# Kernel tuning notes

Hardware: AMD Instinct MI355X
Metric: run time of the kernel (lower is better)

The kernel has to match this reference:

```python
import jax, jax.numpy as jnp
import numpy as np

VOCAB, EMB, HID, LAT = 32000, 512, 1024, 512
B, T = 32, 128


def setup_inputs() -> dict:
    key = jax.random.key(0)
    ks = jax.random.split(key, 10)
    s = 0.02
    return {
        "latent_vector": jax.random.normal(ks[0], (B, LAT), jnp.float32),
        "target_tokens": jax.random.randint(ks[1], (B, T), 0, VOCAB),
        "emb": jax.random.normal(ks[2], (VOCAB, EMB), jnp.float32) * s,
        "W_lh": jax.random.normal(ks[3], (HID, LAT), jnp.float32) * s,
        "b_lh": jnp.zeros((HID,), jnp.float32),
        "W_ih": jax.random.normal(ks[4], (4 * HID, EMB), jnp.float32) * s,
        "b_ih": jnp.zeros((4 * HID,), jnp.float32),
        "W_hh": jax.random.normal(ks[5], (4 * HID, HID), jnp.float32) * s,
        "b_hh": jnp.zeros((4 * HID,), jnp.float32),
        "W_out": jax.random.normal(ks[6], (VOCAB, HID), jnp.float32) * s,
        "b_out": jnp.zeros((VOCAB,), jnp.float32),
    }


def reference(latent_vector, target_tokens, emb, W_lh, b_lh, W_ih, b_ih, W_hh, b_hh, W_out, b_out):
    # teacher_forcing_ratio = 1.0 (deterministic): input at step t is target_tokens[:, t-1]
    h = latent_vector @ W_lh.T + b_lh            # [B, HID]
    c = jnp.zeros_like(h)
    xs = emb[target_tokens[:, :-1]]              # [B, T-1, EMB]
    xs = jnp.swapaxes(xs, 0, 1)                  # [T-1, B, EMB]

    def step(carry, x):
        h, c = carry
        gates = x @ W_ih.T + b_ih + h @ W_hh.T + b_hh   # [B, 4*HID]
        i, f, g, o = jnp.split(gates, 4, axis=-1)       # PyTorch LSTM gate order
        c = jax.nn.sigmoid(f) * c + jax.nn.sigmoid(i) * jnp.tanh(g)
        h = jax.nn.sigmoid(o) * jnp.tanh(c)
        logits = h @ W_out.T + b_out                    # [B, VOCAB]
        return (h, c), logits

    _, logits = jax.lax.scan(step, (h, c), xs)          # [T-1, B, VOCAB]
    return jnp.swapaxes(logits, 0, 1)                   # [B, T-1, VOCAB]
```

## Files before the change

kernel.cpp:

```cpp
#include <hip/hip_runtime.h>
#include <cstdint>

typedef __bf16 bf16x8 __attribute__((ext_vector_type(8)));
typedef __bf16 bf16x4 __attribute__((ext_vector_type(4)));
typedef float  f32x4  __attribute__((ext_vector_type(4)));

#define VOCAB 32000
#define EMB   512
#define HID   1024
#define LAT   512
#define BATCH 32
#define TSTEP 127
#define MROWS 4064
#define MPAD  4096
#define G4    4096
#define NBLK2 64
#define NTM   32
#define NTN   250
#define FSTRIDE 64

__device__ __forceinline__ float sigf(float x){ return 1.0f / (1.0f + __expf(-x)); }
__device__ __forceinline__ float tanhfast(float x){
    float ax = fabsf(x);
    float e  = __expf(-2.0f * ax);
    float t  = (1.0f - e) / (1.0f + e);
    return copysignf(t, x);
}

__device__ __forceinline__ void gll16(void* lds, const void* gsrc){
    __builtin_amdgcn_global_load_lds(
        (const __attribute__((address_space(1))) unsigned int*)gsrc,
        (__attribute__((address_space(3))) unsigned int*)lds,
        16, 0, 0);
}

__global__ __launch_bounds__(256) void init_kernel(
    const float* __restrict__ latent,
    const float* __restrict__ Wlh,
    const float* __restrict__ blh,
    __bf16* __restrict__ h0,
    __bf16* __restrict__ Hall,
    unsigned* __restrict__ flags,
    const float* __restrict__ Whh,
    __bf16* __restrict__ Whhb)
{
    if (blockIdx.x >= 128){
        const int n4 = G4 * HID / 4;
        for (int i = (blockIdx.x - 128) * 256 + threadIdx.x; i < n4; i += 64 * 256){
            float4 v = ((const float4*)Whh)[i];
            bf16x4 o = { (__bf16)v.x, (__bf16)v.y, (__bf16)v.z, (__bf16)v.w };
            ((bf16x4*)Whhb)[i] = o;
        }
        return;
    }
    if (blockIdx.x == 0 && threadIdx.x < 128)
        flags[threadIdx.x * FSTRIDE] = 0u;

    int id = blockIdx.x * 256 + threadIdx.x;
    int b = id >> 10, j = id & 1023;
    float s = blh[j];
    const float4* lr = (const float4*)(latent + (size_t)b * LAT);
    const float4* wr = (const float4*)(Wlh + (size_t)j * LAT);
    for (int k = 0; k < LAT / 4; ++k){
        float4 a = lr[k], w = wr[k];
        s += a.x * w.x + a.y * w.y + a.z * w.z + a.w * w.w;
    }
    h0[id] = (__bf16)s;
    Hall[(size_t)MROWS * HID + id] = (__bf16)0.0f;
}

__global__ __launch_bounds__(256) void gemm_xg(
    const float* __restrict__ emb,
    const float* __restrict__ Wih,
    const int*   __restrict__ tok,
    float*       __restrict__ xg,
    const float* __restrict__ bih,
    const float* __restrict__ bhh)
{
    __shared__ __bf16 As[2][128 * 32];
    __shared__ __bf16 Bs[2][128 * 32];

    const int tid  = threadIdx.x;
    const int wid  = tid >> 6, lane = tid & 63;
    const int tile_n = blockIdx.x, tile_m = blockIdx.y;
    const int wr = wid >> 1, wc = wid & 1;

    f32x4 acc[4][4] = {};

    auto stage = [&](int kt, int buf){
        #pragma unroll
        for (int j = 0; j < 2; ++j){
            const int slot = tid + j * 256;
            const int row  = slot >> 2;
            const int kb   = kt * 32 + (slot & 3) * 8;
            {
                const int brow = tile_n * 128 + row;
                const float4* p = (const float4*)(Wih + (size_t)brow * EMB + kb);
                float4 u = p[0], v = p[1];
                bf16x8 w = { (__bf16)u.x, (__bf16)u.y, (__bf16)u.z, (__bf16)u.w,
                             (__bf16)v.x, (__bf16)v.y, (__bf16)v.z, (__bf16)v.w };
                *(bf16x8*)&Bs[buf][row * 32 + (slot & 3) * 8] = w;
            }
            {
                int r = tile_m * 128 + row;
                int rc = (r < MROWS) ? r : (MROWS - 1);
                int token = tok[(rc & 31) * 128 + (rc >> 5)];
                const float4* p = (const float4*)(emb + (size_t)token * EMB + kb);
                float4 u = p[0], v = p[1];
                bf16x8 w = { (__bf16)u.x, (__bf16)u.y, (__bf16)u.z, (__bf16)u.w,
                             (__bf16)v.x, (__bf16)v.y, (__bf16)v.z, (__bf16)v.w };
                *(bf16x8*)&As[buf][row * 32 + (slot & 3) * 8] = w;
            }
        }
    };

    const int KT = EMB / 32;
    stage(0, 0);
    for (int kt = 0; kt < KT; ++kt){
        const int buf = kt & 1;
        __syncthreads();
        if (kt + 1 < KT) stage(kt + 1, buf ^ 1);
        const __bf16* Abuf = As[buf];
        const __bf16* Bbuf = Bs[buf];
        const int ar = lane & 15, ko = (lane >> 4) * 8;
        bf16x8 av[4], bv[4];
        #pragma unroll
        for (int m = 0; m < 4; ++m)
            av[m] = *(const bf16x8*)&Abuf[(wr * 64 + m * 16 + ar) * 32 + ko];
        #pragma unroll
        for (int n = 0; n < 4; ++n)
            bv[n] = *(const bf16x8*)&Bbuf[(wc * 64 + n * 16 + ar) * 32 + ko];
        #pragma unroll
        for (int m = 0; m < 4; ++m)
            #pragma unroll
            for (int n = 0; n < 4; ++n)
                acc[m][n] = __builtin_amdgcn_mfma_f32_16x16x32_bf16(av[m], bv[n], acc[m][n], 0, 0, 0);
    }

    const int r0 = tile_m * 128 + wr * 64 + ((lane >> 4) << 2);
    const int c0 = tile_n * 128 + wc * 64 + (lane & 15);
    #pragma unroll
    for (int m = 0; m < 4; ++m){
        #pragma unroll
        for (int n = 0; n < 4; ++n){
            const int col = c0 + n * 16;
            float badd = bih[col] + bhh[col];
            #pragma unroll
            for (int q = 0; q < 4; ++q){
                int row = r0 + m * 16 + q;
                xg[(size_t)row * G4 + col] = acc[m][n][q] + badd;
            }
        }
    }
}

template<int BF16B>
__global__ __launch_bounds__(256) void gemm_logits(
    const __bf16* __restrict__ A,
    const float*  __restrict__ Bf,
    const __bf16* __restrict__ Bb,
    float*        __restrict__ C,
    const float*  __restrict__ bias)
{
    __shared__ __bf16 As[2][128 * 32];
    __shared__ __bf16 Bs[2][128 * 32];

    const int tid  = threadIdx.x;
    const int wid  = tid >> 6, lane = tid & 63;
    const int bid = blockIdx.x;
    const int s   = (bid & 7) * (NTM * NTN / 8) + (bid >> 3);
    const int g   = s / (8 * NTN), rem = s % (8 * NTN);
    const int tile_m = g * 8 + (rem & 7);
    const int tile_n = rem >> 3;
    const int wr = wid >> 1, wc = wid & 1;

    f32x4 acc[4][4] = {};

    auto stage = [&](int kt, int buf){
        const int kb = kt * 32 + (lane & 3) * 8;
        #pragma unroll
        for (int c2 = 0; c2 < 2; ++c2){
            int rA = tile_m * 128 + c2 * 64 + wid * 16 + (lane >> 2);
            gll16(&As[buf][c2 * 2048 + wid * 512], A + (size_t)rA * HID + kb);
            if constexpr (BF16B){
                int rB = tile_n * 128 + c2 * 64 + wid * 16 + (lane >> 2);
                gll16(&Bs[buf][c2 * 2048 + wid * 512], Bb + (size_t)rB * HID + kb);
            }
        }
        if constexpr (!BF16B){
            #pragma unroll
            for (int j = 0; j < 2; ++j){
                const int slot = tid + j * 256;
                const int row  = slot >> 2;
                const int kb2  = kt * 32 + (slot & 3) * 8;
                const int brow = tile_n * 128 + row;
                const float4* p = (const float4*)(Bf + (size_t)brow * HID + kb2);
                float4 u = p[0], v = p[1];
                bf16x8 w = { (__bf16)u.x, (__bf16)u.y, (__bf16)u.z, (__bf16)u.w,
                             (__bf16)v.x, (__bf16)v.y, (__bf16)v.z, (__bf16)v.w };
                *(bf16x8*)&Bs[buf][row * 32 + (slot & 3) * 8] = w;
            }
        }
    };

    const int KT = HID / 32;
    stage(0, 0);
    for (int kt = 0; kt < KT; ++kt){
        const int buf = kt & 1;
        __syncthreads();
        if (kt + 1 < KT) stage(kt + 1, buf ^ 1);
        const __bf16* Abuf = As[buf];
        const __bf16* Bbuf = Bs[buf];
        const int ar = lane & 15, ko = (lane >> 4) * 8;
        bf16x8 av[4], bv[4];
        #pragma unroll
        for (int m = 0; m < 4; ++m)
            av[m] = *(const bf16x8*)&Abuf[(wr * 64 + m * 16 + ar) * 32 + ko];
        #pragma unroll
        for (int n = 0; n < 4; ++n)
            bv[n] = *(const bf16x8*)&Bbuf[(wc * 64 + n * 16 + ar) * 32 + ko];
        #pragma unroll
        for (int m = 0; m < 4; ++m)
            #pragma unroll
            for (int n = 0; n < 4; ++n)
                acc[m][n] = __builtin_amdgcn_mfma_f32_16x16x32_bf16(
                    bv[n], av[m], acc[m][n], 0, 0, 0);
    }

    const int r0 = tile_m * 128 + wr * 64 + (lane & 15);
    const int c0 = tile_n * 128 + wc * 64 + ((lane >> 4) << 2);
    #pragma unroll
    for (int m = 0; m < 4; ++m){
        const int row = r0 + m * 16;
        if (row < MROWS){
            const int t = row >> 5, b = row & 31;
            float* crow = &C[((size_t)b * TSTEP + t) * VOCAB];
            #pragma unroll
            for (int n = 0; n < 4; ++n){
                const int col = c0 + n * 16;
                const f32x4 bd = *(const f32x4*)&bias[col];
                f32x4 v = acc[m][n] + bd;
                __builtin_nontemporal_store(v, (f32x4*)&crow[col]);
            }
        }
    }
}

__global__ __launch_bounds__(512) void lstm_coop(
    const float*  __restrict__ xg,
    __bf16*       __restrict__ Hall,
    __bf16*       __restrict__ hbuf,
    const __bf16* __restrict__ Whhb,
    unsigned*     __restrict__ flags,
    const float*  __restrict__ Woutf,
    __bf16*       __restrict__ Woutb)
{
    if (blockIdx.x >= NBLK2){
        if (Woutb){
            const int n4 = VOCAB * HID / 4;
            for (int i = (blockIdx.x - NBLK2) * 512 + threadIdx.x; i < n4; i += 192 * 512){
                float4 v = ((const float4*)Woutf)[i];
                bf16x4 o = { (__bf16)v.x, (__bf16)v.y, (__bf16)v.z, (__bf16)v.w };
                ((bf16x4*)Woutb)[i] = o;
            }
        }
        return;
    }

    __shared__ float lds_g[8 * 8 * 4 * 64];
    const int tid = threadIdx.x, wid = tid >> 6, lane = tid & 63;
    const int jb = blockIdx.x * 16;

    bf16x8 bfrag[4][4];
    {
        const int un = lane & 15, ko = (lane >> 4) * 8;
        #pragma unroll
        for (int cf = 0; cf < 4; ++cf){
            const __bf16* base =
                Whhb + ((size_t)cf * HID + jb + un) * HID + wid * 128 + ko;
            #pragma unroll
            for (int ks = 0; ks < 4; ++ks)
                bfrag[cf][ks] = *(const bf16x8*)(base + ks * 32);
        }
    }

    const int b2 = tid >> 3, up0 = (tid & 7) * 2;
    const int mt2 = b2 >> 4, r2 = b2 & 15, reg2 = r2 & 3, lb2 = (r2 >> 2) << 4;
    float cst[2] = {0.0f, 0.0f};

    const float* xq = xg + (size_t)b2 * G4 + jb + up0;
    float2 xv[4];
    if (tid < 256){
        #pragma unroll
        for (int g = 0; g < 4; ++g) xv[g] = *(const float2*)(xq + g * HID);
    }

    const size_t e0 = (size_t)(lane & 15) * HID + wid * 128 + (lane >> 4) * 8;
    const int pflag = (wid * 8 + (lane & 7)) * FSTRIDE;

    for (int t = 0; t < TSTEP; ++t){
        if (t > 0){
            const unsigned tgt = (unsigned)t;
            for (;;){
                unsigned f = __hip_atomic_load(&flags[pflag],
                                __ATOMIC_RELAXED, __HIP_MEMORY_SCOPE_AGENT);
                if (f >= tgt) break;
                __builtin_amdgcn_s_sleep(1);
            }
        }

        const unsigned long long* hq =
            (const unsigned long long*)(hbuf + (size_t)(t & 1) * (BATCH * HID));
        union { unsigned long long q[2]; bf16x8 v; } xa[8];
        #pragma unroll
        for (int ks = 0; ks < 4; ++ks){
            size_t q0 = (e0 + (size_t)ks * 32) >> 2;
            size_t q1 = q0 + ((size_t)16 * HID >> 2);
            xa[ks].q[0]     = __hip_atomic_load(hq + q0,     __ATOMIC_RELAXED, __HIP_MEMORY_SCOPE_AGENT);
            xa[ks].q[1]     = __hip_atomic_load(hq + q0 + 1, __ATOMIC_RELAXED, __HIP_MEMORY_SCOPE_AGENT);
            xa[4 + ks].q[0] = __hip_atomic_load(hq + q1,     __ATOMIC_RELAXED, __HIP_MEMORY_SCOPE_AGENT);
            xa[4 + ks].q[1] = __hip_atomic_load(hq + q1 + 1, __ATOMIC_RELAXED, __HIP_MEMORY_SCOPE_AGENT);
        }
        f32x4 a[2][4] = {};
        #pragma unroll
        for (int ks = 0; ks < 4; ++ks){
            #pragma unroll
            for (int cf = 0; cf < 4; ++cf){
                a[0][cf] = __builtin_amdgcn_mfma_f32_16x16x32_bf16(xa[ks].v,     bfrag[cf][ks], a[0][cf], 0, 0, 0);
                a[1][cf] = __builtin_amdgcn_mfma_f32_16x16x32_bf16(xa[4 + ks].v, bfrag[cf][ks], a[1][cf], 0, 0, 0);
            }
        }
        #pragma unroll
        for (int bh = 0; bh < 2; ++bh)
            #pragma unroll
            for (int cf = 0; cf < 4; ++cf)
                #pragma unroll
                for (int q = 0; q < 4; ++q)
                    lds_g[((((bh * 4 + cf) * 8 + wid) * 4) + q) * 64 + lane] = a[bh][cf][q];
        __syncthreads();

        unsigned pku = 0;
        if (tid < 256){
            const float* xn = xq + (size_t)(t + 1) * (BATCH * G4);
            float2 xnew[4];
            #pragma unroll
            for (int g = 0; g < 4; ++g) xnew[g] = *(const float2*)(xn + g * HID);

            float h2[2];
            #pragma unroll
            for (int du = 0; du < 2; ++du){
                int u2 = up0 + du;
                float gate[4];
                #pragma unroll
                for (int ty = 0; ty < 4; ++ty){
                    int li = lb2 | u2;
                    float s = 0.0f;
                    #pragma unroll
                    for (int w = 0; w < 8; ++w)
                        s += lds_g[((((mt2 * 4 + ty) * 8 + w) * 4) + reg2) * 64 + li];
                    gate[ty] = s;
                }
                float gi = gate[0] + ((du == 0) ? xv[0].x : xv[0].y);
                float gf = gate[1] + ((du == 0) ? xv[1].x : xv[1].y);
                float gc = gate[2] + ((du == 0) ? xv[2].x : xv[2].y);
                float go = gate[3] + ((du == 0) ? xv[3].x : xv[3].y);
                float c = sigf(gf) * cst[du] + sigf(gi) * tanhfast(gc);
                cst[du] = c;
                h2[du] = sigf(go) * tanhfast(c);
            }
            #pragma unroll
            for (int g = 0; g < 4; ++g) xv[g] = xnew[g];

            union { __bf16 h[2]; unsigned u; } pk;
            pk.h[0] = (__bf16)h2[0]; pk.h[1] = (__bf16)h2[1];
            pku = pk.u;
            unsigned* hw = (unsigned*)(hbuf + (size_t)((t + 1) & 1) * (BATCH * HID)
                                       + (size_t)b2 * HID + jb + up0);
            __hip_atomic_store(hw, pku, __ATOMIC_RELAXED, __HIP_MEMORY_SCOPE_AGENT);
        }

        if (t + 1 == TSTEP){
            if (tid < 256)
                *(unsigned*)(Hall + ((size_t)t * BATCH + b2) * HID + jb + up0) = pku;
            break;
        }

        __syncthreads();
        if (tid == 0)
            __hip_atomic_store(&flags[blockIdx.x * FSTRIDE], (unsigned)(t + 1),
                               __ATOMIC_RELAXED, __HIP_MEMORY_SCOPE_AGENT);
        if (tid < 256)
            *(unsigned*)(Hall + ((size_t)t * BATCH + b2) * HID + jb + up0) = pku;
    }
}

extern "C" void kernel_launch(void* const* d_in, const int* in_sizes, int n_in,
                              void* d_out, int out_size, void* d_ws, size_t ws_size,
                              hipStream_t stream)
{
    const float* latent = (const float*)d_in[0];
    const int*   tokens = (const int*)d_in[1];
    const float* emb    = (const float*)d_in[2];
    const float* Wlh    = (const float*)d_in[3];
    const float* blh    = (const float*)d_in[4];
    const float* Wih    = (const float*)d_in[5];
    const float* bih    = (const float*)d_in[6];
    const float* Whh    = (const float*)d_in[7];
    const float* bhh    = (const float*)d_in[8];
    const float* Wout   = (const float*)d_in[9];
    const float* bout   = (const float*)d_in[10];
    float* out = (float*)d_out;

    const size_t xg_b   = (size_t)MPAD * G4 * 4;
    const size_t hall_b = (size_t)MPAD * HID * 2;
    const size_t whh_b  = (size_t)G4 * HID * 2;
    const size_t wout_b = (size_t)VOCAB * HID * 2;
    const size_t hb_b   = (size_t)2 * BATCH * HID * 2;
    const size_t cnt_b  = (size_t)128 * FSTRIDE * 4;

    char* p = (char*)d_ws;
    const bool wsA = ws_size >= xg_b + hall_b + whh_b + wout_b + hb_b + cnt_b;
    const bool wsB = ws_size >= hall_b + whh_b + wout_b + hb_b + cnt_b;

    float* xg;
    if (wsA){ xg = (float*)p; p += xg_b; }
    else    { xg = (float*)d_out; }
    __bf16* Hall = (__bf16*)p; p += hall_b;
    __bf16* Whhb = (__bf16*)p; p += whh_b;
    __bf16* Woutb = nullptr;
    if (wsA || wsB){ Woutb = (__bf16*)p; p += wout_b; }
    __bf16* hbuf = (__bf16*)p; p += hb_b;
    unsigned* flags = (unsigned*)p; p += cnt_b;

    init_kernel<<<dim3(192), dim3(256), 0, stream>>>(
        latent, Wlh, blh, hbuf, Hall, flags, Whh, Whhb);

    gemm_xg<<<dim3(G4 / 128, MPAD / 128), dim3(256), 0, stream>>>(
        emb, Wih, tokens, xg, bih, bhh);

    {
        const float*  xgc   = xg;
        __bf16*       hallp = Hall;
        __bf16*       hbp   = hbuf;
        const __bf16* whhp  = Whhb;
        unsigned*     flagp = flags;
        const float*  wof   = Wout;
        __bf16*       wob   = Woutb;
        void* args[] = { (void*)&xgc, (void*)&hallp, (void*)&hbp, (void*)&whhp,
                         (void*)&flagp, (void*)&wof, (void*)&wob };
        (void)hipLaunchCooperativeKernel((void*)lstm_coop, dim3(256), dim3(512),
                                         args, 0, stream);
    }

    if (Woutb)
        gemm_logits<1><<<dim3(NTM * NTN), dim3(256), 0, stream>>>(
            Hall, (const float*)nullptr, Woutb, out, bout);
    else
        gemm_logits<0><<<dim3(NTM * NTN), dim3(256), 0, stream>>>(
            Hall, Wout, (const __bf16*)nullptr, out, bout);
}
```

Before: 1.187 ms.

## Replace per-block step flags with tagged hidden-state words for LSTM sync

Result: slower. 1.774 ms (+49.5%).

```diff
diff --git a/kernel.cpp b/kernel.cpp
--- a/kernel.cpp
+++ b/kernel.cpp
@@ -17,7 +17,7 @@
 #define NBLK2 64
 #define NTM   32
 #define NTN   250
-#define FSTRIDE 64
+#define HWORDS 16384
 
 __device__ __forceinline__ float sigf(float x){ return 1.0f / (1.0f + __expf(-x)); }
 __device__ __forceinline__ float tanhfast(float x){
@@ -33,14 +33,14 @@
         (__attribute__((address_space(3))) unsigned int*)lds,
         16, 0, 0);
 }
+__device__ __forceinline__ void bar(){ asm volatile("s_barrier" ::: "memory"); }
 
 __global__ __launch_bounds__(256) void init_kernel(
     const float* __restrict__ latent,
     const float* __restrict__ Wlh,
     const float* __restrict__ blh,
-    __bf16* __restrict__ h0,
+    unsigned long long* __restrict__ hbt,
     __bf16* __restrict__ Hall,
-    unsigned* __restrict__ flags,
     const float* __restrict__ Whh,
     __bf16* __restrict__ Whhb)
 {
@@ -53,8 +53,6 @@
         }
         return;
     }
-    if (blockIdx.x == 0 && threadIdx.x < 128)
-        flags[threadIdx.x * FSTRIDE] = 0u;
 
     int id = blockIdx.x * 256 + threadIdx.x;
     int b = id >> 10, j = id & 1023;
@@ -65,7 +63,14 @@
         float4 a = lr[k], w = wr[k];
         s += a.x * w.x + a.y * w.y + a.z * w.z + a.w * w.w;
     }
-    h0[id] = (__bf16)s;
+    float s_hi = __shfl_down(s, 1);
+    if ((j & 1) == 0){
+        union { __bf16 h[2]; unsigned u; } pk;
+        pk.h[0] = (__bf16)s; pk.h[1] = (__bf16)s_hi;
+        hbt[(size_t)b * 512 + (j >> 1)] = (unsigned long long)pk.u;
+    }
+    if (id < HWORDS)
+        hbt[HWORDS + id] = 0xFFFFFFFF00000000ULL;
     Hall[(size_t)MROWS * HID + id] = (__bf16)0.0f;
 }
 
@@ -247,13 +252,12 @@
 }
 
 __global__ __launch_bounds__(512) void lstm_coop(
-    const float*  __restrict__ xg,
-    __bf16*       __restrict__ Hall,
-    __bf16*       __restrict__ hbuf,
-    const __bf16* __restrict__ Whhb,
-    unsigned*     __restrict__ flags,
-    const float*  __restrict__ Woutf,
-    __bf16*       __restrict__ Woutb)
+    const float*        __restrict__ xg,
+    __bf16*             __restrict__ Hall,
+    unsigned long long* __restrict__ hbt,
+    const __bf16*       __restrict__ Whhb,
+    const float*        __restrict__ Woutf,
+    __bf16*             __restrict__ Woutb)
 {
     if (blockIdx.x >= NBLK2){
         if (Woutb){
@@ -295,39 +299,48 @@
         for (int g = 0; g < 4; ++g) xv[g] = *(const float2*)(xq + g * HID);
     }
 
-    const size_t e0 = (size_t)(lane & 15) * HID + wid * 128 + (lane >> 4) * 8;
-    const int pflag = (wid * 8 + (lane & 7)) * FSTRIDE;
+    const size_t i0 = (size_t)(lane & 15) * 512 + wid * 64 + (lane >> 4) * 4;
+    const size_t wwr = (size_t)b2 * 512 + jb / 2 + (tid & 7);
 
     for (int t = 0; t < TSTEP; ++t){
-        if (t > 0){
-            const unsigned tgt = (unsigned)t;
-            for (;;){
-                unsigned f = __hip_atomic_load(&flags[pflag],
-                                __ATOMIC_RELAXED, __HIP_MEMORY_SCOPE_AGENT);
-                if (f >= tgt) break;
-                __builtin_amdgcn_s_sleep(1);
-            }
-        }
-
-        const unsigned long long* hq =
-            (const unsigned long long*)(hbuf + (size_t)(t & 1) * (BATCH * HID));
-        union { unsigned long long q[2]; bf16x8 v; } xa[8];
+        const unsigned long long* tb = hbt + (size_t)(t & 1) * HWORDS;
+        const unsigned tagv = (unsigned)t;
+        unsigned long long w[2][4][4];
+        for (;;){
+            #pragma unroll
+            for (int bh = 0; bh < 2; ++bh)
+                #pragma unroll
+                for (int ks = 0; ks < 4; ++ks)
+                    #pragma unroll
+                    for (int c = 0; c < 4; ++c)
+                        w[bh][ks][c] = __hip_atomic_load(
+                            tb + i0 + (size_t)bh * (16 * 512) + ks * 16 + c,
+                            __ATOMIC_RELAXED, __HIP_MEMORY_SCOPE_AGENT);
+            unsigned bad = 0;
+            #pragma unroll
+            for (int bh = 0; bh < 2; ++bh)
+                #pragma unroll
+                for (int ks = 0; ks < 4; ++ks)
+                    #pragma unroll
+                    for (int c = 0; c < 4; ++c)
+                        bad |= ((unsigned)(w[bh][ks][c] >> 32)) ^ tagv;
+            if (!bad) break;
+            __builtin_amdgcn_s_sleep(1);
+        }
+
+        f32x4 a[2][4] = {};
         #pragma unroll
         for (int ks = 0; ks < 4; ++ks){
-            size_t q0 = (e0 + (size_t)ks * 32) >> 2;
-            size_t q1 = q0 + ((size_t)16 * HID >> 2);
-            xa[ks].q[0]     = __hip_atomic_load(hq + q0,     __ATOMIC_RELAXED, __HIP_MEMORY_SCOPE_AGENT);
-            xa[ks].q[1]     = __hip_atomic_load(hq + q0 + 1, __ATOMIC_RELAXED, __HIP_MEMORY_SCOPE_AGENT);
-            xa[4 + ks].q[0] = __hip_atomic_load(hq + q1,     __ATOMIC_RELAXED, __HIP_MEMORY_SCOPE_AGENT);
-            xa[4 + ks].q[1] = __hip_atomic_load(hq + q1 + 1, __ATOMIC_RELAXED, __HIP_MEMORY_SCOPE_AGENT);
-        }
-        f32x4 a[2][4] = {};
-        #pragma unroll
-        for (int ks = 0; ks < 4; ++ks){
+            union { unsigned p[4]; bf16x8 v; } f0, f1;
+            #pragma unroll
+            for (int c = 0; c < 4; ++c){
+                f0.p[c] = (unsigned)w[0][ks][c];
+                f1.p[c] = (unsigned)w[1][ks][c];
+            }
             #pragma unroll
             for (int cf = 0; cf < 4; ++cf){
-                a[0][cf] = __builtin_amdgcn_mfma_f32_16x16x32_bf16(xa[ks].v,     bfrag[cf][ks], a[0][cf], 0, 0, 0);
-                a[1][cf] = __builtin_amdgcn_mfma_f32_16x16x32_bf16(xa[4 + ks].v, bfrag[cf][ks], a[1][cf], 0, 0, 0);
+                a[0][cf] = __builtin_amdgcn_mfma_f32_16x16x32_bf16(f0.v, bfrag[cf][ks], a[0][cf], 0, 0, 0);
+                a[1][cf] = __builtin_amdgcn_mfma_f32_16x16x32_bf16(f1.v, bfrag[cf][ks], a[1][cf], 0, 0, 0);
             }
         }
         #pragma unroll
@@ -339,7 +352,6 @@
                     lds_g[((((bh * 4 + cf) * 8 + wid) * 4) + q) * 64 + lane] = a[bh][cf][q];
         __syncthreads();
 
-        unsigned pku = 0;
         if (tid < 256){
             const float* xn = xq + (size_t)(t + 1) * (BATCH * G4);
             float2 xnew[4];
@@ -356,8 +368,8 @@
                     int li = lb2 | u2;
                     float s = 0.0f;
                     #pragma unroll
-                    for (int w = 0; w < 8; ++w)
-                        s += lds_g[((((mt2 * 4 + ty) * 8 + w) * 4) + reg2) * 64 + li];
+                    for (int w8 = 0; w8 < 8; ++w8)
+                        s += lds_g[((((mt2 * 4 + ty) * 8 + w8) * 4) + reg2) * 64 + li];
                     gate[ty] = s;
                 }
                 float gi = gate[0] + ((du == 0) ? xv[0].x : xv[0].y);
@@ -373,24 +385,17 @@
 
             union { __bf16 h[2]; unsigned u; } pk;
             pk.h[0] = (__bf16)h2[0]; pk.h[1] = (__bf16)h2[1];
-            pku = pk.u;
-            unsigned* hw = (unsigned*)(hbuf + (size_t)((t + 1) & 1) * (BATCH * HID)
-                                       + (size_t)b2 * HID + jb + up0);
-            __hip_atomic_store(hw, pku, __ATOMIC_RELAXED, __HIP_MEMORY_SCOPE_AGENT);
-        }
-
-        if (t + 1 == TSTEP){
-            if (tid < 256)
-                *(unsigned*)(Hall + ((size_t)t * BATCH + b2) * HID + jb + up0) = pku;
-            break;
-        }
-
-        __syncthreads();
-        if (tid == 0)
-            __hip_atomic_store(&flags[blockIdx.x * FSTRIDE], (unsigned)(t + 1),
-                               __ATOMIC_RELAXED, __HIP_MEMORY_SCOPE_AGENT);
-        if (tid < 256)
-            *(unsigned*)(Hall + ((size_t)t * BATCH + b2) * HID + jb + up0) = pku;
+            if (t + 1 < TSTEP){
+                unsigned long long wv =
+                    ((unsigned long long)(unsigned)(t + 1) << 32) | (unsigned long long)pk.u;
+                __hip_atomic_store(hbt + (size_t)((t + 1) & 1) * HWORDS + wwr, wv,
+                                   __ATOMIC_RELAXED, __HIP_MEMORY_SCOPE_AGENT);
+            }
+            *(unsigned*)(Hall + ((size_t)t * BATCH + b2) * HID + jb + up0) = pk.u;
+        }
+
+        if (t + 1 == TSTEP) break;
+        bar();
     }
 }
 
@@ -415,12 +420,11 @@
     const size_t hall_b = (size_t)MPAD * HID * 2;
     const size_t whh_b  = (size_t)G4 * HID * 2;
     const size_t wout_b = (size_t)VOCAB * HID * 2;
-    const size_t hb_b   = (size_t)2 * BATCH * HID * 2;
-    const size_t cnt_b  = (size_t)128 * FSTRIDE * 4;
+    const size_t hbt_b  = (size_t)2 * HWORDS * 8;
 
     char* p = (char*)d_ws;
-    const bool wsA = ws_size >= xg_b + hall_b + whh_b + wout_b + hb_b + cnt_b;
-    const bool wsB = ws_size >= hall_b + whh_b + wout_b + hb_b + cnt_b;
+    const bool wsA = ws_size >= xg_b + hall_b + whh_b + wout_b + hbt_b;
+    const bool wsB = ws_size >= hall_b + whh_b + wout_b + hbt_b;
 
     float* xg;
     if (wsA){ xg = (float*)p; p += xg_b; }
@@ -429,25 +433,23 @@
     __bf16* Whhb = (__bf16*)p; p += whh_b;
     __bf16* Woutb = nullptr;
     if (wsA || wsB){ Woutb = (__bf16*)p; p += wout_b; }
-    __bf16* hbuf = (__bf16*)p; p += hb_b;
-    unsigned* flags = (unsigned*)p; p += cnt_b;
+    unsigned long long* hbt = (unsigned long long*)p; p += hbt_b;
 
     init_kernel<<<dim3(192), dim3(256), 0, stream>>>(
-        latent, Wlh, blh, hbuf, Hall, flags, Whh, Whhb);
+        latent, Wlh, blh, hbt, Hall, Whh, Whhb);
 
     gemm_xg<<<dim3(G4 / 128, MPAD / 128), dim3(256), 0, stream>>>(
         emb, Wih, tokens, xg, bih, bhh);
 
     {
-        const float*  xgc   = xg;
-        __bf16*       hallp = Hall;
-        __bf16*       hbp   = hbuf;
-        const __bf16* whhp  = Whhb;
-        unsigned*     flagp = flags;
-        const float*  wof   = Wout;
-        __bf16*       wob   = Woutb;
+        const float*        xgc   = xg;
+        __bf16*             hallp = Hall;
+        unsigned long long* hbp   = hbt;
+        const __bf16*       whhp  = Whhb;
+        const float*        wof   = Wout;
+        __bf16*             wob   = Woutb;
         void* args[] = { (void*)&xgc, (void*)&hallp, (void*)&hbp, (void*)&whhp,
-                         (void*)&flagp, (void*)&wof, (void*)&wob };
+                         (void*)&wof, (void*)&wob };
         (void)hipLaunchCooperativeKernel((void*)lstm_coop, dim3(256), dim3(512),
                                          args, 0, stream);
     }
```
